# Optimization experiments

Measured on AMD Instinct MI355X. Metric: run time of the kernel, lower is better.

## Reference

```python
import jax, jax.numpy as jnp
import numpy as np

SEQ_LEN, BATCH, D_IN, D_H, D_OUT = 512, 64, 1024, 1024, 1024
W_SCALE = 0.02  # small init so sigmoid/tanh stay in a sane range


def setup_inputs() -> dict:
    key = jax.random.key(0)
    ks = jax.random.split(key, 12)
    rn = lambda k, shape: jax.random.normal(k, shape, dtype=jnp.float32)
    return {
        "x_seq": rn(ks[0], (SEQ_LEN, BATCH, D_IN)),
        "h0": jnp.zeros((BATCH, D_H), dtype=jnp.float32),
        "Wxz_w": rn(ks[1], (D_H, D_IN)) * W_SCALE,
        "Wxz_b": rn(ks[2], (D_H,)) * W_SCALE,
        "Whz_w": rn(ks[3], (D_H, D_H)) * W_SCALE,
        "Wxr_w": rn(ks[4], (D_H, D_IN)) * W_SCALE,
        "Wxr_b": rn(ks[5], (D_H,)) * W_SCALE,
        "Whr_w": rn(ks[6], (D_H, D_H)) * W_SCALE,
        "Wxn_w": rn(ks[7], (D_H, D_IN)) * W_SCALE,
        "Wxn_b": rn(ks[8], (D_H,)) * W_SCALE,
        "Whn_w": rn(ks[9], (D_H, D_H)) * W_SCALE,
        "Why_w": rn(ks[10], (D_OUT, D_H)) * W_SCALE,
        "Why_b": rn(ks[11], (D_OUT,)) * W_SCALE,
    }


def reference(x_seq, h0, Wxz_w, Wxz_b, Whz_w, Wxr_w, Wxr_b, Whr_w,
              Wxn_w, Wxn_b, Whn_w, Why_w, Why_b):
    # Precompute all input projections in one batched GEMM per gate:
    # (S, B, D_in) @ (D_in, D_h) -> (S, B, D_h). torch Linear: x @ W.T + b.
    xz = jnp.einsum('sbi,hi->sbh', x_seq, Wxz_w) + Wxz_b
    xr = jnp.einsum('sbi,hi->sbh', x_seq, Wxr_w) + Wxr_b
    xn = jnp.einsum('sbi,hi->sbh', x_seq, Wxn_w) + Wxn_b

    def step(h, xs):
        xz_t, xr_t, xn_t = xs
        z = jax.nn.sigmoid(xz_t + h @ Whz_w.T)
        r = jax.nn.sigmoid(xr_t + h @ Whr_w.T)
        n = jnp.tanh(xn_t + (r * h) @ Whn_w.T)
        h_new = (1.0 - z) * h + z * n
        return h_new, h_new

    h_last, hs = jax.lax.scan(step, h0, (xz, xr, xn))  # hs: (S, B, D_h)
    outputs = jnp.einsum('sbh,oh->sbo', hs, Why_w) + Why_b
    return outputs, h_last
```

## Files before the change

kernel.cpp:

```cpp
#include <hip/hip_runtime.h>

typedef unsigned int uint;
typedef unsigned short ushort;

typedef short s8v __attribute__((ext_vector_type(8)));
typedef float f4v __attribute__((ext_vector_type(4)));

#define S_LEN 512
#define BATCH 64
#define DH    1024
#define DIN   1024

union B8 { s8v v; uint u[4]; unsigned long long ull[2]; ushort s[8]; };

__device__ inline ushort f2bf(float f){
  uint u = __builtin_bit_cast(uint, f);
  u += 0x7fffu + ((u >> 16) & 1u);
  return (ushort)(u >> 16);
}
__device__ inline float bf2f(ushort s){
  uint u = ((uint)s) << 16;
  return __builtin_bit_cast(float, u);
}

__device__ inline f4v mfma16(s8v a, s8v b, f4v c){
  return __builtin_amdgcn_mfma_f32_16x16x32_bf16(a, b, c, 0, 0, 0);
}

__device__ inline s8v ld_b8(const ushort* p){
  return *reinterpret_cast<const s8v*>(p);
}

__device__ inline s8v ld_b8_llc(const ushort* p){
  B8 b;
  const unsigned long long* q = (const unsigned long long*)p;
  b.ull[0] = __hip_atomic_load(q,   __ATOMIC_RELAXED, __HIP_MEMORY_SCOPE_AGENT);
  b.ull[1] = __hip_atomic_load(q+1, __ATOMIC_RELAXED, __HIP_MEMORY_SCOPE_AGENT);
  return b.v;
}

__device__ inline s8v cvt8(float4 a, float4 b){
  B8 r;
  r.s[0]=f2bf(a.x); r.s[1]=f2bf(a.y); r.s[2]=f2bf(a.z); r.s[3]=f2bf(a.w);
  r.s[4]=f2bf(b.x); r.s[5]=f2bf(b.y); r.s[6]=f2bf(b.z); r.s[7]=f2bf(b.w);
  return r.v;
}

__global__ void cvt_kernel(const float* __restrict__ src, ushort* __restrict__ dst, int n){
  int i = (blockIdx.x * blockDim.x + threadIdx.x) * 4;
  if (i + 3 < n){
    float4 v = *reinterpret_cast<const float4*>(src + i);
    unsigned long long p = (unsigned long long)f2bf(v.x)
                         | ((unsigned long long)f2bf(v.y) << 16)
                         | ((unsigned long long)f2bf(v.z) << 32)
                         | ((unsigned long long)f2bf(v.w) << 48);
    *reinterpret_cast<unsigned long long*>(dst + i) = p;
  }
}

__global__ void __launch_bounds__(256, 1)
proj3_kernel(const float* __restrict__ X,
             const ushort* __restrict__ W0, const ushort* __restrict__ W1, const ushort* __restrict__ W2,
             const float* __restrict__ bias0, const float* __restrict__ bias1, const float* __restrict__ bias2,
             ushort* __restrict__ C0, ushort* __restrict__ C1, ushort* __restrict__ C2)
{
  const int lane = threadIdx.x & 63;
  const int wave = threadIdx.x >> 6;
  const int l15  = lane & 15;
  const int krow = (lane >> 4) << 3;
  const int n0 = blockIdx.x * 64;
  const int m0 = blockIdx.y * 128 + wave * 32;

  const ushort* Ws[3] = {W0, W1, W2};
  const float*  Bs[3] = {bias0, bias1, bias2};
  ushort*       Cs[3] = {C0, C1, C2};

  f4v acc[2][3][4];
  #pragma unroll
  for (int ms = 0; ms < 2; ++ms)
    #pragma unroll
    for (int g = 0; g < 3; ++g)
      #pragma unroll
      for (int nn = 0; nn < 4; ++nn)
        acc[ms][g][nn] = (f4v){0.f,0.f,0.f,0.f};

  const float* a0 = X + (m0 + l15) * DIN + krow;
  const float* a1 = a0 + 16 * DIN;

  for (int k = 0; k < DIN; k += 32){
    s8v af[2];
    {
      const float4* p0 = reinterpret_cast<const float4*>(a0 + k);
      const float4* p1 = reinterpret_cast<const float4*>(a1 + k);
      af[0] = cvt8(p0[0], p0[1]);
      af[1] = cvt8(p1[0], p1[1]);
    }
    #pragma unroll
    for (int g = 0; g < 3; ++g){
      const ushort* W = Ws[g];
      #pragma unroll
      for (int nn = 0; nn < 4; ++nn){
        s8v bfr = ld_b8(W + (n0 + nn*16 + l15) * DIN + k + krow);
        acc[0][g][nn] = mfma16(af[0], bfr, acc[0][g][nn]);
        acc[1][g][nn] = mfma16(af[1], bfr, acc[1][g][nn]);
      }
    }
  }

  #pragma unroll
  for (int g = 0; g < 3; ++g){
    ushort* C = Cs[g];
    #pragma unroll
    for (int nn = 0; nn < 4; ++nn){
      const int n = n0 + nn*16 + l15;
      const float bv = Bs[g][n];
      #pragma unroll
      for (int ms = 0; ms < 2; ++ms){
        #pragma unroll
        for (int r = 0; r < 4; ++r){
          int m = m0 + ms*16 + ((lane>>4)<<2) + r;
          C[m * DH + n] = f2bf(acc[ms][g][nn][r] + bv);
        }
      }
    }
  }
}

__global__ void __launch_bounds__(256, 1)
gemm1_kernel(const ushort* __restrict__ A, const ushort* __restrict__ W,
             const float* __restrict__ bias, float* __restrict__ C)
{
  const int lane = threadIdx.x & 63;
  const int wave = threadIdx.x >> 6;
  const int l15  = lane & 15;
  const int krow = (lane >> 4) << 3;
  const int n0 = blockIdx.x * 128;
  const int m0 = blockIdx.y * 128 + wave * 32;

  f4v acc[2][8];
  #pragma unroll
  for (int ms = 0; ms < 2; ++ms)
    #pragma unroll
    for (int nn = 0; nn < 8; ++nn)
      acc[ms][nn] = (f4v){0.f,0.f,0.f,0.f};

  const ushort* a0 = A + (m0 + l15) * DH + krow;
  const ushort* a1 = a0 + 16 * DH;

  for (int k = 0; k < DH; k += 32){
    s8v af0 = ld_b8(a0 + k);
    s8v af1 = ld_b8(a1 + k);
    #pragma unroll
    for (int nn = 0; nn < 8; ++nn){
      s8v b = ld_b8(W + (n0 + nn*16 + l15) * DH + k + krow);
      acc[0][nn] = mfma16(af0, b, acc[0][nn]);
      acc[1][nn] = mfma16(af1, b, acc[1][nn]);
    }
  }

  #pragma unroll
  for (int nn = 0; nn < 8; ++nn){
    const int n = n0 + nn*16 + l15;
    const float bv = bias[n];
    #pragma unroll
    for (int ms = 0; ms < 2; ++ms){
      #pragma unroll
      for (int r = 0; r < 4; ++r){
        int m = m0 + ms*16 + ((lane>>4)<<2) + r;
        C[m * DH + n] = acc[ms][nn][r] + bv;
      }
    }
  }
}

__global__ void __launch_bounds__(256, 1)
scan_kernel(const ushort* __restrict__ xz, const ushort* __restrict__ xr,
            const ushort* __restrict__ xn,
            const ushort* __restrict__ Whz, const ushort* __restrict__ Whr,
            const ushort* __restrict__ Whn,
            const float* __restrict__ h0,
            ushort* __restrict__ hbuf,
            ushort* __restrict__ rhbuf,
            ushort* __restrict__ hs,
            float*  __restrict__ hlast,
            uint* __restrict__ hflags,
            uint* __restrict__ rhflags)
{
  const int tid  = threadIdx.x;
  const int wid  = blockIdx.x;
  const int g    = wid >> 6;
  const int jt   = wid & 63;
  const int b0   = g * 16;
  const int j0   = jt * 16;
  const int wave = tid >> 6;
  const int lane = tid & 63;
  const int l15  = lane & 15;
  const int krow = (lane >> 4) << 3;
  const int kbase = wave * 256;

  s8v wz[8], wr[8], wn[8];
  {
    const int wrow = j0 + l15;
    #pragma unroll
    for (int kk = 0; kk < 8; ++kk){
      int off = wrow * DH + kbase + kk*32 + krow;
      wz[kk] = ld_b8(Whz + off);
      wr[kk] = ld_b8(Whr + off);
      wn[kk] = ld_b8(Whn + off);
    }
  }

  const int bl = tid >> 4;
  const int jl = tid & 15;
  const int brow = b0 + bl;
  const int jcol = j0 + jl;
  const int arow = b0 + l15;

  __shared__ float red[8][256];

  float h = h0[brow * DH + jcol];
  {
    ushort mybf = f2bf(h);
    uint other = (uint)(ushort)__shfl_xor((int)mybf, 1, 64);
    if ((tid & 1) == 0){
      uint pack = (uint)mybf | (other << 16);
      uint* dst = (uint*)(hbuf + 64*1024 + brow*DH + jcol);
      __hip_atomic_store(dst, pack, __ATOMIC_RELAXED, __HIP_MEMORY_SCOPE_AGENT);
    }
  }
  __syncthreads();
  if (tid == 0)
    __hip_atomic_store(&hflags[wid*4], 1u, __ATOMIC_RELAXED, __HIP_MEMORY_SCOPE_AGENT);

  float zreg = 0.f;

  #pragma unroll 1
  for (int t = 0; t < S_LEN; ++t){
    {
      const uint* fp = hflags + (g*64 + wave*16 + l15) * 4;
      const uint tgt = (uint)(t + 1);
      while (true){
        uint v = __hip_atomic_load(fp, __ATOMIC_RELAXED, __HIP_MEMORY_SCOPE_AGENT);
        if (__all(v >= tgt)) break;
        __builtin_amdgcn_s_sleep(2);
      }
    }
    __asm__ volatile("" ::: "memory");

    const int xidx = (t * BATCH + brow) * DH + jcol;
    float xzv = bf2f(xz[xidx]);
    float xrv = bf2f(xr[xidx]);

    f4v accz = (f4v){0.f,0.f,0.f,0.f};
    f4v accr = (f4v){0.f,0.f,0.f,0.f};
    {
      const ushort* ap = hbuf + ((t ^ 1) & 1) * (64*1024) + arow * DH + kbase + krow;
      #pragma unroll
      for (int kk = 0; kk < 8; ++kk){
        s8v a = ld_b8_llc(ap + kk*32);
        accz = mfma16(a, wz[kk], accz);
        accr = mfma16(a, wr[kk], accr);
      }
    }
    {
      int base = ((lane >> 4) * 4) * 16 + l15;
      #pragma unroll
      for (int r = 0; r < 4; ++r){
        red[wave][base + r*16]   = accz[r];
        red[4+wave][base + r*16] = accr[r];
      }
    }
    __syncthreads();
    float sz = red[0][tid] + red[1][tid] + red[2][tid] + red[3][tid];
    float sr = red[4][tid] + red[5][tid] + red[6][tid] + red[7][tid];
    float z = 1.f / (1.f + __expf(-(xzv + sz)));
    float r = 1.f / (1.f + __expf(-(xrv + sr)));
    zreg = z;
    float rh = r * h;
    {
      ushort mybf = f2bf(rh);
      uint other = (uint)(ushort)__shfl_xor((int)mybf, 1, 64);
      if ((tid & 1) == 0){
        uint pack = (uint)mybf | (other << 16);
        uint* dst = (uint*)(rhbuf + (t & 1)*(64*1024) + brow*DH + jcol);
        __hip_atomic_store(dst, pack, __ATOMIC_RELAXED, __HIP_MEMORY_SCOPE_AGENT);
      }
    }
    __syncthreads();
    if (tid == 0)
      __hip_atomic_store(&rhflags[wid*4], (uint)(t+1), __ATOMIC_RELAXED, __HIP_MEMORY_SCOPE_AGENT);

    {
      const uint* fp = rhflags + (g*64 + wave*16 + l15) * 4;
      const uint tgt = (uint)(t + 1);
      while (true){
        uint v = __hip_atomic_load(fp, __ATOMIC_RELAXED, __HIP_MEMORY_SCOPE_AGENT);
        if (__all(v >= tgt)) break;
        __builtin_amdgcn_s_sleep(2);
      }
    }
    __asm__ volatile("" ::: "memory");

    float xnv = bf2f(xn[xidx]);
    f4v accn = (f4v){0.f,0.f,0.f,0.f};
    {
      const ushort* ap = rhbuf + (t & 1)*(64*1024) + arow * DH + kbase + krow;
      #pragma unroll
      for (int kk = 0; kk < 8; ++kk){
        s8v a = ld_b8_llc(ap + kk*32);
        accn = mfma16(a, wn[kk], accn);
      }
    }
    {
      int base = ((lane >> 4) * 4) * 16 + l15;
      #pragma unroll
      for (int r4 = 0; r4 < 4; ++r4)
        red[wave][base + r4*16] = accn[r4];
    }
    __syncthreads();
    float sn = red[0][tid] + red[1][tid] + red[2][tid] + red[3][tid];
    float pre = xnv + sn;
    float e = __expf(2.f * pre);
    float n = 1.f - 2.f / (e + 1.f);
    float hnew = h + zreg * (n - h);
    h = hnew;
    {
      ushort mybf = f2bf(hnew);
      uint other = (uint)(ushort)__shfl_xor((int)mybf, 1, 64);
      if ((tid & 1) == 0){
        uint pack = (uint)mybf | (other << 16);
        uint* dst = (uint*)(hbuf + (t & 1)*(64*1024) + brow*DH + jcol);
        __hip_atomic_store(dst, pack, __ATOMIC_RELAXED, __HIP_MEMORY_SCOPE_AGENT);
      }
      hs[xidx] = mybf;
      if (t == S_LEN-1) hlast[brow*DH + jcol] = hnew;
    }
    __syncthreads();
    if (tid == 0)
      __hip_atomic_store(&hflags[wid*4], (uint)(t+2), __ATOMIC_RELAXED, __HIP_MEMORY_SCOPE_AGENT);
  }
}

extern "C" void kernel_launch(void* const* d_in, const int* in_sizes, int n_in,
                              void* d_out, int out_size, void* d_ws, size_t ws_size,
                              hipStream_t stream) {
  const float* x_seq = (const float*)d_in[0];
  const float* h0    = (const float*)d_in[1];
  const float* Wxz_w = (const float*)d_in[2];
  const float* Wxz_b = (const float*)d_in[3];
  const float* Whz_w = (const float*)d_in[4];
  const float* Wxr_w = (const float*)d_in[5];
  const float* Wxr_b = (const float*)d_in[6];
  const float* Whr_w = (const float*)d_in[7];
  const float* Wxn_w = (const float*)d_in[8];
  const float* Wxn_b = (const float*)d_in[9];
  const float* Whn_w = (const float*)d_in[10];
  const float* Why_w = (const float*)d_in[11];
  const float* Why_b = (const float*)d_in[12];

  const size_t MiB = 1u << 20;
  unsigned char* ws = (unsigned char*)d_ws;

  ushort* Whz16 = (ushort*)(ws + 0*MiB);
  ushort* Whr16 = (ushort*)(ws + 2*MiB);
  ushort* Whn16 = (ushort*)(ws + 4*MiB);
  ushort* Wxz16 = (ushort*)(ws + 6*MiB);
  ushort* Wxr16 = (ushort*)(ws + 8*MiB);
  ushort* Wxn16 = (ushort*)(ws + 10*MiB);
  ushort* Why16 = (ushort*)(ws + 12*MiB);
  ushort* xn_buf = (ushort*)(ws + 16*MiB);
  ushort* hs     = (ushort*)(ws + 80*MiB);
  ushort* hbuf   = (ushort*)(ws + 144*MiB);
  ushort* rhbuf  = (ushort*)(ws + 144*MiB + 256*1024);
  uint*   hflags = (uint*)  (ws + 144*MiB + 512*1024);
  uint*   rhflags= (uint*)  (ws + 144*MiB + 516*1024);

  ushort* xz_buf = (ushort*)d_out;
  ushort* xr_buf = xz_buf + (size_t)S_LEN*BATCH*DH;
  float*  out_f  = (float*)d_out;
  float*  hlast  = out_f + (size_t)S_LEN*BATCH*DH;

  const int NW = DH * DIN;

  cvt_kernel<<<1024, 256, 0, stream>>>(Whz_w, Whz16, NW);
  cvt_kernel<<<1024, 256, 0, stream>>>(Whr_w, Whr16, NW);
  cvt_kernel<<<1024, 256, 0, stream>>>(Whn_w, Whn16, NW);
  cvt_kernel<<<1024, 256, 0, stream>>>(Wxz_w, Wxz16, NW);
  cvt_kernel<<<1024, 256, 0, stream>>>(Wxr_w, Wxr16, NW);
  cvt_kernel<<<1024, 256, 0, stream>>>(Wxn_w, Wxn16, NW);
  cvt_kernel<<<1024, 256, 0, stream>>>(Why_w, Why16, NW);

  proj3_kernel<<<dim3(16, 256), 256, 0, stream>>>(
      x_seq, Wxz16, Wxr16, Wxn16, Wxz_b, Wxr_b, Wxn_b, xz_buf, xr_buf, xn_buf);

  hipMemsetAsync((void*)hflags, 0, 8192, stream);

  scan_kernel<<<256, 256, 0, stream>>>(
      xz_buf, xr_buf, xn_buf, Whz16, Whr16, Whn16, h0,
      hbuf, rhbuf, hs, hlast, hflags, rhflags);

  gemm1_kernel<<<dim3(8, 256), 256, 0, stream>>>(hs, Why16, Why_b, out_f);
}
```

Measured before the change: 6.332 ms.

## Replace flag-based scan sync with versioned bf16 hidden-state words, pre-convert X

Each hidden and reset-gated value in the scan is now stored as a 32-bit word holding the bf16 payload and a 16-bit step version. Consumers poll the data itself until every version matches. This removes the separate flag stores, flag polling and the trailing barrier each step, and it drops the flag memset. Separately, x_seq is converted to bf16 once (into the hs buffer) so the projection GEMM loads bf16 directly instead of converting per tile. In exchange, the exchange buffers double in size, the polling loop rereads 32 words per retry, and the conversion adds an extra pass over x_seq.

New measurement: 8.935 ms. +41.1%, slower.

```diff
diff --git a/kernel.cpp b/kernel.cpp
--- a/kernel.cpp
+++ b/kernel.cpp
@@ -29,21 +29,6 @@
 
 __device__ inline s8v ld_b8(const ushort* p){
   return *reinterpret_cast<const s8v*>(p);
-}
-
-__device__ inline s8v ld_b8_llc(const ushort* p){
-  B8 b;
-  const unsigned long long* q = (const unsigned long long*)p;
-  b.ull[0] = __hip_atomic_load(q,   __ATOMIC_RELAXED, __HIP_MEMORY_SCOPE_AGENT);
-  b.ull[1] = __hip_atomic_load(q+1, __ATOMIC_RELAXED, __HIP_MEMORY_SCOPE_AGENT);
-  return b.v;
-}
-
-__device__ inline s8v cvt8(float4 a, float4 b){
-  B8 r;
-  r.s[0]=f2bf(a.x); r.s[1]=f2bf(a.y); r.s[2]=f2bf(a.z); r.s[3]=f2bf(a.w);
-  r.s[4]=f2bf(b.x); r.s[5]=f2bf(b.y); r.s[6]=f2bf(b.z); r.s[7]=f2bf(b.w);
-  return r.v;
 }
 
 __global__ void cvt_kernel(const float* __restrict__ src, ushort* __restrict__ dst, int n){
@@ -59,7 +44,7 @@
 }
 
 __global__ void __launch_bounds__(256, 1)
-proj3_kernel(const float* __restrict__ X,
+proj3_kernel(const ushort* __restrict__ A16,
              const ushort* __restrict__ W0, const ushort* __restrict__ W1, const ushort* __restrict__ W2,
              const float* __restrict__ bias0, const float* __restrict__ bias1, const float* __restrict__ bias2,
              ushort* __restrict__ C0, ushort* __restrict__ C1, ushort* __restrict__ C2)
@@ -84,25 +69,20 @@
       for (int nn = 0; nn < 4; ++nn)
         acc[ms][g][nn] = (f4v){0.f,0.f,0.f,0.f};
 
-  const float* a0 = X + (m0 + l15) * DIN + krow;
-  const float* a1 = a0 + 16 * DIN;
+  const ushort* a0 = A16 + (m0 + l15) * DIN + krow;
+  const ushort* a1 = a0 + 16 * DIN;
 
   for (int k = 0; k < DIN; k += 32){
-    s8v af[2];
-    {
-      const float4* p0 = reinterpret_cast<const float4*>(a0 + k);
-      const float4* p1 = reinterpret_cast<const float4*>(a1 + k);
-      af[0] = cvt8(p0[0], p0[1]);
-      af[1] = cvt8(p1[0], p1[1]);
-    }
+    s8v af0 = ld_b8(a0 + k);
+    s8v af1 = ld_b8(a1 + k);
     #pragma unroll
     for (int g = 0; g < 3; ++g){
       const ushort* W = Ws[g];
       #pragma unroll
       for (int nn = 0; nn < 4; ++nn){
         s8v bfr = ld_b8(W + (n0 + nn*16 + l15) * DIN + k + krow);
-        acc[0][g][nn] = mfma16(af[0], bfr, acc[0][g][nn]);
-        acc[1][g][nn] = mfma16(af[1], bfr, acc[1][g][nn]);
+        acc[0][g][nn] = mfma16(af0, bfr, acc[0][g][nn]);
+        acc[1][g][nn] = mfma16(af1, bfr, acc[1][g][nn]);
       }
     }
   }
@@ -173,18 +153,56 @@
   }
 }
 
+__device__ inline void st_ver(uint* p, float v, uint ver){
+  uint pack = ((uint)f2bf(v)) | (ver << 16);
+  __hip_atomic_store(p, pack, __ATOMIC_RELAXED, __HIP_MEMORY_SCOPE_AGENT);
+}
+
+__device__ inline void poll_load8(const uint* base, uint ver, s8v out8[8]){
+  const uint vp = ver | (ver << 16);
+  while (true){
+    unsigned long long q[32];
+    #pragma unroll
+    for (int kk = 0; kk < 8; ++kk){
+      const unsigned long long* p = (const unsigned long long*)(base + kk*32);
+      q[kk*4+0] = __hip_atomic_load(p+0, __ATOMIC_RELAXED, __HIP_MEMORY_SCOPE_AGENT);
+      q[kk*4+1] = __hip_atomic_load(p+1, __ATOMIC_RELAXED, __HIP_MEMORY_SCOPE_AGENT);
+      q[kk*4+2] = __hip_atomic_load(p+2, __ATOMIC_RELAXED, __HIP_MEMORY_SCOPE_AGENT);
+      q[kk*4+3] = __hip_atomic_load(p+3, __ATOMIC_RELAXED, __HIP_MEMORY_SCOPE_AGENT);
+    }
+    uint m = 0;
+    #pragma unroll
+    for (int i = 0; i < 32; ++i){
+      uint lo = (uint)q[i], hi = (uint)(q[i] >> 32);
+      m |= (__builtin_amdgcn_perm(hi, lo, 0x07060302u) ^ vp);
+    }
+    if (__all(m == 0)){
+      #pragma unroll
+      for (int kk = 0; kk < 8; ++kk){
+        B8 r;
+        #pragma unroll
+        for (int i = 0; i < 4; ++i){
+          uint lo = (uint)q[kk*4+i], hi = (uint)(q[kk*4+i] >> 32);
+          r.u[i] = __builtin_amdgcn_perm(hi, lo, 0x05040100u);
+        }
+        out8[kk] = r.v;
+      }
+      return;
+    }
+    __builtin_amdgcn_s_sleep(1);
+  }
+}
+
 __global__ void __launch_bounds__(256, 1)
 scan_kernel(const ushort* __restrict__ xz, const ushort* __restrict__ xr,
             const ushort* __restrict__ xn,
             const ushort* __restrict__ Whz, const ushort* __restrict__ Whr,
             const ushort* __restrict__ Whn,
             const float* __restrict__ h0,
-            ushort* __restrict__ hbuf,
-            ushort* __restrict__ rhbuf,
+            uint* __restrict__ hv,
+            uint* __restrict__ rhv,
             ushort* __restrict__ hs,
-            float*  __restrict__ hlast,
-            uint* __restrict__ hflags,
-            uint* __restrict__ rhflags)
+            float*  __restrict__ hlast)
 {
   const int tid  = threadIdx.x;
   const int wid  = blockIdx.x;
@@ -216,128 +234,64 @@
   const int jcol = j0 + jl;
   const int arow = b0 + l15;
 
-  __shared__ float red[8][256];
+  __shared__ float redA[8][256];
+  __shared__ float redB[4][256];
 
   float h = h0[brow * DH + jcol];
-  {
-    ushort mybf = f2bf(h);
-    uint other = (uint)(ushort)__shfl_xor((int)mybf, 1, 64);
-    if ((tid & 1) == 0){
-      uint pack = (uint)mybf | (other << 16);
-      uint* dst = (uint*)(hbuf + 64*1024 + brow*DH + jcol);
-      __hip_atomic_store(dst, pack, __ATOMIC_RELAXED, __HIP_MEMORY_SCOPE_AGENT);
-    }
-  }
-  __syncthreads();
-  if (tid == 0)
-    __hip_atomic_store(&hflags[wid*4], 1u, __ATOMIC_RELAXED, __HIP_MEMORY_SCOPE_AGENT);
+  st_ver(hv + 1*(64*1024) + brow*DH + jcol, h, 0u);
 
   float zreg = 0.f;
+  const int rbase = ((lane >> 4) * 4) * 16 + l15;
 
   #pragma unroll 1
   for (int t = 0; t < S_LEN; ++t){
-    {
-      const uint* fp = hflags + (g*64 + wave*16 + l15) * 4;
-      const uint tgt = (uint)(t + 1);
-      while (true){
-        uint v = __hip_atomic_load(fp, __ATOMIC_RELAXED, __HIP_MEMORY_SCOPE_AGENT);
-        if (__all(v >= tgt)) break;
-        __builtin_amdgcn_s_sleep(2);
-      }
-    }
-    __asm__ volatile("" ::: "memory");
-
     const int xidx = (t * BATCH + brow) * DH + jcol;
-    float xzv = bf2f(xz[xidx]);
-    float xrv = bf2f(xr[xidx]);
+    ushort xzr = xz[xidx];
+    ushort xrr = xr[xidx];
+    ushort xnr = xn[xidx];
+
+    s8v af[8];
+    poll_load8(hv + ((t & 1) ^ 1)*(64*1024) + arow*DH + kbase + krow, (uint)t, af);
 
     f4v accz = (f4v){0.f,0.f,0.f,0.f};
     f4v accr = (f4v){0.f,0.f,0.f,0.f};
-    {
-      const ushort* ap = hbuf + ((t ^ 1) & 1) * (64*1024) + arow * DH + kbase + krow;
-      #pragma unroll
-      for (int kk = 0; kk < 8; ++kk){
-        s8v a = ld_b8_llc(ap + kk*32);
-        accz = mfma16(a, wz[kk], accz);
-        accr = mfma16(a, wr[kk], accr);
-      }
-    }
-    {
-      int base = ((lane >> 4) * 4) * 16 + l15;
-      #pragma unroll
-      for (int r = 0; r < 4; ++r){
-        red[wave][base + r*16]   = accz[r];
-        red[4+wave][base + r*16] = accr[r];
-      }
+    #pragma unroll
+    for (int kk = 0; kk < 8; ++kk){
+      accz = mfma16(af[kk], wz[kk], accz);
+      accr = mfma16(af[kk], wr[kk], accr);
+    }
+    #pragma unroll
+    for (int r = 0; r < 4; ++r){
+      redA[wave][rbase + r*16]   = accz[r];
+      redA[4+wave][rbase + r*16] = accr[r];
     }
     __syncthreads();
-    float sz = red[0][tid] + red[1][tid] + red[2][tid] + red[3][tid];
-    float sr = red[4][tid] + red[5][tid] + red[6][tid] + red[7][tid];
-    float z = 1.f / (1.f + __expf(-(xzv + sz)));
-    float r = 1.f / (1.f + __expf(-(xrv + sr)));
+    float sz = redA[0][tid] + redA[1][tid] + redA[2][tid] + redA[3][tid];
+    float sr = redA[4][tid] + redA[5][tid] + redA[6][tid] + redA[7][tid];
+    float z = 1.f / (1.f + __expf(-(bf2f(xzr) + sz)));
+    float r = 1.f / (1.f + __expf(-(bf2f(xrr) + sr)));
     zreg = z;
-    float rh = r * h;
-    {
-      ushort mybf = f2bf(rh);
-      uint other = (uint)(ushort)__shfl_xor((int)mybf, 1, 64);
-      if ((tid & 1) == 0){
-        uint pack = (uint)mybf | (other << 16);
-        uint* dst = (uint*)(rhbuf + (t & 1)*(64*1024) + brow*DH + jcol);
-        __hip_atomic_store(dst, pack, __ATOMIC_RELAXED, __HIP_MEMORY_SCOPE_AGENT);
-      }
-    }
+    st_ver(rhv + (t & 1)*(64*1024) + brow*DH + jcol, r * h, (uint)(t + 1));
+
+    poll_load8(rhv + (t & 1)*(64*1024) + arow*DH + kbase + krow, (uint)(t + 1), af);
+
+    f4v accn = (f4v){0.f,0.f,0.f,0.f};
+    #pragma unroll
+    for (int kk = 0; kk < 8; ++kk)
+      accn = mfma16(af[kk], wn[kk], accn);
+    #pragma unroll
+    for (int r4 = 0; r4 < 4; ++r4)
+      redB[wave][rbase + r4*16] = accn[r4];
     __syncthreads();
-    if (tid == 0)
-      __hip_atomic_store(&rhflags[wid*4], (uint)(t+1), __ATOMIC_RELAXED, __HIP_MEMORY_SCOPE_AGENT);
-
-    {
-      const uint* fp = rhflags + (g*64 + wave*16 + l15) * 4;
-      const uint tgt = (uint)(t + 1);
-      while (true){
-        uint v = __hip_atomic_load(fp, __ATOMIC_RELAXED, __HIP_MEMORY_SCOPE_AGENT);
-        if (__all(v >= tgt)) break;
-        __builtin_amdgcn_s_sleep(2);
-      }
-    }
-    __asm__ volatile("" ::: "memory");
-
-    float xnv = bf2f(xn[xidx]);
-    f4v accn = (f4v){0.f,0.f,0.f,0.f};
-    {
-      const ushort* ap = rhbuf + (t & 1)*(64*1024) + arow * DH + kbase + krow;
-      #pragma unroll
-      for (int kk = 0; kk < 8; ++kk){
-        s8v a = ld_b8_llc(ap + kk*32);
-        accn = mfma16(a, wn[kk], accn);
-      }
-    }
-    {
-      int base = ((lane >> 4) * 4) * 16 + l15;
-      #pragma unroll
-      for (int r4 = 0; r4 < 4; ++r4)
-        red[wave][base + r4*16] = accn[r4];
-    }
-    __syncthreads();
-    float sn = red[0][tid] + red[1][tid] + red[2][tid] + red[3][tid];
-    float pre = xnv + sn;
+    float sn = redB[0][tid] + redB[1][tid] + redB[2][tid] + redB[3][tid];
+    float pre = bf2f(xnr) + sn;
     float e = __expf(2.f * pre);
     float n = 1.f - 2.f / (e + 1.f);
     float hnew = h + zreg * (n - h);
     h = hnew;
-    {
-      ushort mybf = f2bf(hnew);
-      uint other = (uint)(ushort)__shfl_xor((int)mybf, 1, 64);
-      if ((tid & 1) == 0){
-        uint pack = (uint)mybf | (other << 16);
-        uint* dst = (uint*)(hbuf + (t & 1)*(64*1024) + brow*DH + jcol);
-        __hip_atomic_store(dst, pack, __ATOMIC_RELAXED, __HIP_MEMORY_SCOPE_AGENT);
-      }
-      hs[xidx] = mybf;
-      if (t == S_LEN-1) hlast[brow*DH + jcol] = hnew;
-    }
-    __syncthreads();
-    if (tid == 0)
-      __hip_atomic_store(&hflags[wid*4], (uint)(t+2), __ATOMIC_RELAXED, __HIP_MEMORY_SCOPE_AGENT);
+    st_ver(hv + (t & 1)*(64*1024) + brow*DH + jcol, hnew, (uint)(t + 1));
+    hs[xidx] = f2bf(hnew);
+    if (t == S_LEN-1) hlast[brow*DH + jcol] = hnew;
   }
 }
 
@@ -370,10 +324,9 @@
   ushort* Why16 = (ushort*)(ws + 12*MiB);
   ushort* xn_buf = (ushort*)(ws + 16*MiB);
   ushort* hs     = (ushort*)(ws + 80*MiB);
-  ushort* hbuf   = (ushort*)(ws + 144*MiB);
-  ushort* rhbuf  = (ushort*)(ws + 144*MiB + 256*1024);
-  uint*   hflags = (uint*)  (ws + 144*MiB + 512*1024);
-  uint*   rhflags= (uint*)  (ws + 144*MiB + 516*1024);
+  ushort* X16    = hs;
+  uint*   hv     = (uint*)  (ws + 144*MiB);
+  uint*   rhv    = (uint*)  (ws + 144*MiB + 512*1024);
 
   ushort* xz_buf = (ushort*)d_out;
   ushort* xr_buf = xz_buf + (size_t)S_LEN*BATCH*DH;
@@ -381,6 +334,7 @@
   float*  hlast  = out_f + (size_t)S_LEN*BATCH*DH;
 
   const int NW = DH * DIN;
+  const int NX = S_LEN * BATCH * DIN;
 
   cvt_kernel<<<1024, 256, 0, stream>>>(Whz_w, Whz16, NW);
   cvt_kernel<<<1024, 256, 0, stream>>>(Whr_w, Whr16, NW);
@@ -389,15 +343,14 @@
   cvt_kernel<<<1024, 256, 0, stream>>>(Wxr_w, Wxr16, NW);
   cvt_kernel<<<1024, 256, 0, stream>>>(Wxn_w, Wxn16, NW);
   cvt_kernel<<<1024, 256, 0, stream>>>(Why_w, Why16, NW);
+  cvt_kernel<<<32768, 256, 0, stream>>>(x_seq, X16, NX);
 
   proj3_kernel<<<dim3(16, 256), 256, 0, stream>>>(
-      x_seq, Wxz16, Wxr16, Wxn16, Wxz_b, Wxr_b, Wxn_b, xz_buf, xr_buf, xn_buf);
-
-  hipMemsetAsync((void*)hflags, 0, 8192, stream);
+      X16, Wxz16, Wxr16, Wxn16, Wxz_b, Wxr_b, Wxn_b, xz_buf, xr_buf, xn_buf);
 
   scan_kernel<<<256, 256, 0, stream>>>(
       xz_buf, xr_buf, xn_buf, Whz16, Whr16, Whn16, h0,
-      hbuf, rhbuf, hs, hlast, hflags, rhflags);
+      hv, rhv, hs, hlast);
 
   gemm1_kernel<<<dim3(8, 256), 256, 0, stream>>>(hs, Why16, Why_b, out_f);
 }
```
